# Optimization experiments

Hardware: AMD Instinct MI355X
Metric: run time of the kernel (lower is better)

The kernel has to match this reference:

```python
import jax, jax.numpy as jnp
import numpy as np

G = 8          # grid_size
N = G * G      # 64 nodes
DEG = 17       # neighbors per node for 8x8 sudoku (2x4 boxes)
STEPS = 32
H = 96         # hidden_dim
E = 16         # embed_size
B = 16         # batch


def sudoku_edges():
    # row (7) + col (7) + 2x4 box (7) neighbors, set-union -> 17 per node
    idx = np.arange(N).reshape(G, G)
    nb = []
    for j in range(N):
        r, c = j // G, j % G
        br, bc = (r // 2) * 2, (c // 4) * 4
        s = set(idx[r, :].tolist()) | set(idx[:, c].tolist()) | set(idx[br:br + 2, bc:bc + 4].flatten().tolist())
        s.discard(j)
        nb.append(sorted(s))
    return np.asarray(nb, dtype=np.int32)  # [64, 17]


def setup_inputs() -> dict:
    key = jax.random.key(0)
    ks = jax.random.split(key, 16)
    sc = 0.05
    inp = {
        "x": jax.random.randint(ks[0], (B, G, G), 0, G + 1),            # given digits, 0 = blank
        "target": jax.random.randint(ks[1], (B, G, G), 0, G) + 1,       # solutions in 1..8
        "edges": jnp.asarray(sudoku_edges()),                            # [64, 17] int32
        "digit_emb": jax.random.normal(ks[2], (G + 1, E), jnp.float32) * sc,
        "row_emb": jax.random.normal(ks[3], (G, E), jnp.float32) * sc,
        "col_emb": jax.random.normal(ks[4], (G, E), jnp.float32) * sc,
        "in0_W": jax.random.normal(ks[5], (3 * E, H), jnp.float32) * sc,
        "in0_b": jnp.zeros((H,), jnp.float32),
        "in_Ws": jax.random.normal(ks[6], (3, H, H), jnp.float32) * sc,
        "in_bs": jnp.zeros((3, H), jnp.float32),
        "msg0_W": jax.random.normal(ks[7], (2 * H, H), jnp.float32) * sc,
        "msg0_b": jnp.zeros((H,), jnp.float32),
        "msg_Ws": jax.random.normal(ks[8], (3, H, H), jnp.float32) * sc,
        "msg_bs": jnp.zeros((3, H), jnp.float32),
        "W_ih": jax.random.normal(ks[9], (2 * H, 4 * H), jnp.float32) * sc,
        "W_hh": jax.random.normal(ks[10], (H, 4 * H), jnp.float32) * sc,
        "b_ih": jnp.zeros((4 * H,), jnp.float32),
        "b_hh": jnp.zeros((4 * H,), jnp.float32),
        "pred_W": jax.random.normal(ks[11], (H, G), jnp.float32) * sc,
        "pred_b": jnp.zeros((G,), jnp.float32),
    }
    return inp


def _mlp(z, W0, b0, Ws, bs):
    # Linear -> ReLU -> Linear -> ReLU -> Linear -> ReLU -> Linear (def_MLP)
    z = jax.nn.relu(z @ W0 + b0)
    z = jax.nn.relu(z @ Ws[0] + bs[0])
    z = jax.nn.relu(z @ Ws[1] + bs[1])
    return z @ Ws[2] + bs[2]


def reference(x, target, edges, digit_emb, row_emb, col_emb,
              in0_W, in0_b, in_Ws, in_bs,
              msg0_W, msg0_b, msg_Ws, msg_bs,
              W_ih, W_hh, b_ih, b_hh, pred_W, pred_b):
    bsz = x.shape[0]
    xf = x.reshape(bsz, N)
    tgt = target.reshape(bsz, N) - 1                      # labels 0..7

    de = digit_emb[xf]                                    # [B,64,E]
    re = row_emb[jnp.repeat(jnp.arange(G), G)]            # [64,E]
    ce = col_emb[jnp.tile(jnp.arange(G), G)]              # [64,E]
    feat = jnp.concatenate([de,
                            jnp.broadcast_to(re[None], (bsz, N, E)),
                            jnp.broadcast_to(ce[None], (bsz, N, E))], axis=-1)
    xin = _mlp(feat, in0_W, in0_b, in_Ws, in_bs)          # [B,64,H]

    h0 = jnp.zeros((bsz, N, H), jnp.float32)
    s0 = jnp.zeros((bsz * N, H), jnp.float32)

    def step(carry, _):
        h, s, loss = carry
        # gather-by-edge message passing
        h_edges = h[:, edges]                                             # [B,64,17,H]
        h_self = jnp.broadcast_to(h[:, :, None, :], (bsz, N, DEG, H))
        msg = _mlp(jnp.concatenate([h_edges, h_self], -1),
                   msg0_W, msg0_b, msg_Ws, msg_bs).sum(axis=2)            # [B,64,H]
        # LSTMCell update
        lstm_in = jnp.concatenate([msg, xin], -1).reshape(bsz * N, 2 * H)
        gates = lstm_in @ W_ih + b_ih + h.reshape(bsz * N, H) @ W_hh + b_hh
        i, f, g, o = jnp.split(gates, 4, axis=-1)
        s2 = jax.nn.sigmoid(f) * s + jax.nn.sigmoid(i) * jnp.tanh(g)
        h2 = (jax.nn.sigmoid(o) * jnp.tanh(s2)).reshape(bsz, N, H)
        # per-step prediction / loss / accuracy
        logp = jax.nn.log_softmax(h2 @ pred_W + pred_b, axis=-1)          # [B,64,8]
        pred = jnp.argmax(logp, axis=-1)
        acc = jnp.mean(jnp.all(pred == tgt, axis=1).astype(jnp.float32))
        loss_n = -jnp.sum(jnp.take_along_axis(logp, tgt[..., None], -1)) / (bsz * N)
        return (h2, s2, loss + loss_n), acc

    (h, s, loss), accs = jax.lax.scan(step, (h0, s0, jnp.float32(0.0)), None, length=STEPS)
    loss = loss / STEPS
    final_pred = jnp.argmax(h @ pred_W + pred_b, axis=-1)                 # [B,64]
    return loss, accs, final_pred
```

## Files before the change

kernel.cpp:

```cpp
#include <hip/hip_runtime.h>

#define DEG 17
#define NSTEPS 32
#define HD 96
#define BB 16
#define NN 64
#define NODES (BB*NN)
#define Z1STR 80
#define Z2STR 84

#define WS_H      0
#define WS_S      98304
#define WS_U0     196608
#define WS_U1     393216
#define WS_XIN    590352
#define WS_GX     688656
#define WS_W1P    1081872
#define WS_W2P    1094160
#define WS_LOSSP  1106448
#define WS_CNTP   1114640

__global__ void wpad_kernel(const float* __restrict__ msg_Ws,
                            float* __restrict__ W1p, float* __restrict__ W2p)
{
  const int k = blockIdx.x;
  const int tid = threadIdx.x;
  const int jg = tid >> 3, jj = tid & 7;
  float v1 = 0.f, v2 = 0.f;
  if (jj < 6) {
    v1 = msg_Ws[k*96 + jg*6 + jj];
    v2 = msg_Ws[9216 + k*96 + jg*6 + jj];
  }
  W1p[k*128 + tid] = v1;
  W2p[k*128 + tid] = v2;
}

__global__ void init_kernel(
    const int* __restrict__ x,
    const float* __restrict__ digit_emb,
    const float* __restrict__ row_emb,
    const float* __restrict__ col_emb,
    const float* __restrict__ in0_W,
    const float* __restrict__ in0_b,
    const float* __restrict__ in_Ws,
    const float* __restrict__ in_bs,
    float* __restrict__ xin)
{
  const int node = blockIdx.x;
  const int j = threadIdx.x;
  const int n = node & 63;
  const int r = n >> 3, c = n & 7;
  __shared__ float feat[48];
  __shared__ float za[HD];
  __shared__ float zb[HD];
  if (j < 16)      feat[j] = digit_emb[x[node]*16 + j];
  else if (j < 32) feat[j] = row_emb[r*16 + (j-16)];
  else if (j < 48) feat[j] = col_emb[c*16 + (j-32)];
  __syncthreads();
  float a = in0_b[j];
  for (int k = 0; k < 48; ++k) a = fmaf(feat[k], in0_W[k*HD + j], a);
  za[j] = fmaxf(a, 0.f);
  __syncthreads();
  a = in_bs[j];
  for (int k = 0; k < HD; ++k) a = fmaf(za[k], in_Ws[k*HD + j], a);
  zb[j] = fmaxf(a, 0.f);
  __syncthreads();
  a = in_bs[HD + j];
  for (int k = 0; k < HD; ++k) a = fmaf(zb[k], in_Ws[9216 + k*HD + j], a);
  za[j] = fmaxf(a, 0.f);
  __syncthreads();
  a = in_bs[2*HD + j];
  for (int k = 0; k < HD; ++k) a = fmaf(za[k], in_Ws[2*9216 + k*HD + j], a);
  xin[node*HD + j] = a;
}

__global__ __launch_bounds__(384) void gx_kernel(
    const float* __restrict__ xin, const float* __restrict__ W_ih,
    const float* __restrict__ b_ih, const float* __restrict__ b_hh,
    float* __restrict__ gx)
{
  __shared__ float xs[4*HD];
  const int tid = threadIdx.x;
  const int base = blockIdx.x * 4;
  {
    const int m = tid / HD, k = tid - m*HD;
    xs[m*HD + k] = xin[(base+m)*HD + k];
  }
  __syncthreads();
  const int j = tid;
  float a0 = b_ih[j] + b_hh[j], a1 = a0, a2 = a0, a3 = a0;
  for (int k = 0; k < HD; ++k) {
    const float w = W_ih[(96+k)*384 + j];
    a0 = fmaf(xs[k], w, a0);
    a1 = fmaf(xs[HD+k], w, a1);
    a2 = fmaf(xs[2*HD+k], w, a2);
    a3 = fmaf(xs[3*HD+k], w, a3);
  }
  gx[(base+0)*384 + j] = a0;
  gx[(base+1)*384 + j] = a1;
  gx[(base+2)*384 + j] = a2;
  gx[(base+3)*384 + j] = a3;
}

__global__ __launch_bounds__(384) void step_kernel(
    const float* __restrict__ u_prev, float* __restrict__ u_next,
    float* __restrict__ h, float* __restrict__ s,
    const float* __restrict__ gx,
    const int* __restrict__ edges,
    const float* __restrict__ W1p, const float* __restrict__ W2p,
    const float* __restrict__ msg0_W, const float* __restrict__ msg0_b,
    const float* __restrict__ msg_Ws, const float* __restrict__ msg_bs,
    const float* __restrict__ W_ih, const float* __restrict__ W_hh,
    const float* __restrict__ pred_W, const float* __restrict__ pred_b,
    const int* __restrict__ target,
    float* __restrict__ lossP, int* __restrict__ cntP,
    float* __restrict__ final_pred_out, int step)
{
  __shared__ float sm[15744];
  float* const z1s = sm;
  float* const z2s = sm + 7680;
  float* const s3t   = sm;
  float* const msgh  = sm + 384;
  float* const h2t   = sm + 1152;
  float* const lgt   = sm + 1536;
  float* const gates = sm + 1568;
  float* const P3    = sm + 3104;
  float* const PL = z2s;
  float* const PU = z2s;

  const int tid = threadIdx.x;
  const int blk = blockIdx.x;
  const int base = blk * 4;
  const int bb = blk >> 4;
  const int nbase = (blk & 15) * 4;

  {
    const int m = tid / HD, k = tid - m*HD;
    const float usv = u_prev[(base+m)*192 + 96 + k];
    const float b0v = msg0_b[k];
    z1s[k*Z1STR + m*20 + 17] = 0.f;
    z1s[k*Z1STR + m*20 + 18] = 0.f;
    z1s[k*Z1STR + m*20 + 19] = 0.f;
    const int erow = (nbase + m) * DEG;
    #pragma unroll 1
    for (int r = 0; r < DEG; ++r) {
      const int nbr = edges[erow + r];
      const float ue = u_prev[(bb*64 + nbr)*192 + k];
      z1s[k*Z1STR + m*20 + r] = fmaxf(ue + usv + b0v, 0.f);
    }
  }
  __syncthreads();

  if (tid < 320) {
    const int jg = tid & 15, dg = tid >> 4;
    const int j6 = jg*6, j8 = jg*8, dg4 = dg*4;
    float acc[4][6];
    #pragma unroll
    for (int dd = 0; dd < 4; ++dd)
      #pragma unroll
      for (int jj = 0; jj < 6; ++jj) acc[dd][jj] = 0.f;
    #pragma unroll 4
    for (int k = 0; k < HD; ++k) {
      const float4 z = *(const float4*)&z1s[k*Z1STR + dg4];
      const float* wp = W1p + k*128 + j8;
      const float4 wa = *(const float4*)wp;
      const float2 wb = *(const float2*)(wp + 4);
      const float ze[4] = {z.x, z.y, z.z, z.w};
      const float we[6] = {wa.x, wa.y, wa.z, wa.w, wb.x, wb.y};
      #pragma unroll
      for (int dd = 0; dd < 4; ++dd)
        #pragma unroll
        for (int jj = 0; jj < 6; ++jj)
          acc[dd][jj] = fmaf(ze[dd], we[jj], acc[dd][jj]);
    }
    #pragma unroll
    for (int jj = 0; jj < 6; ++jj) {
      const float b1 = msg_bs[j6 + jj];
      float4 q;
      q.x = fmaxf(acc[0][jj] + b1, 0.f);
      q.y = fmaxf(acc[1][jj] + b1, 0.f);
      q.z = fmaxf(acc[2][jj] + b1, 0.f);
      q.w = fmaxf(acc[3][jj] + b1, 0.f);
      *(float4*)&z2s[(j6+jj)*Z2STR + dg4] = q;
    }
  }
  __syncthreads();

  {
    s3t[tid] = 0.f;
    const int m = tid / HD, k = tid - m*HD;
    msgh[(96+k)*4 + m] = h[(base+m)*HD + k];
  }
  __syncthreads();

  if (tid < 320) {
    const int jg = tid & 15, dg = tid >> 4;
    const int j6 = jg*6, j8 = jg*8, dg4 = dg*4;
    const int nd = dg / 5, dgl = dg - nd*5;
    float acc[4][6];
    #pragma unroll
    for (int dd = 0; dd < 4; ++dd)
      #pragma unroll
      for (int jj = 0; jj < 6; ++jj) acc[dd][jj] = 0.f;
    #pragma unroll 4
    for (int k = 0; k < HD; ++k) {
      const float4 z = *(const float4*)&z2s[k*Z2STR + dg4];
      const float* wp = W2p + k*128 + j8;
      const float4 wa = *(const float4*)wp;
      const float2 wb = *(const float2*)(wp + 4);
      const float ze[4] = {z.x, z.y, z.z, z.w};
      const float we[6] = {wa.x, wa.y, wa.z, wa.w, wb.x, wb.y};
      #pragma unroll
      for (int dd = 0; dd < 4; ++dd)
        #pragma unroll
        for (int jj = 0; jj < 6; ++jj)
          acc[dd][jj] = fmaf(ze[dd], we[jj], acc[dd][jj]);
    }
    const int nvalid = (dgl < 4) ? 4 : 1;
    #pragma unroll
    for (int jj = 0; jj < 6; ++jj) {
      const float b2 = msg_bs[96 + j6 + jj];
      float p = 0.f;
      #pragma unroll
      for (int dd = 0; dd < 4; ++dd)
        if (dd < nvalid) p += fmaxf(acc[dd][jj] + b2, 0.f);
      atomicAdd(&s3t[(j6+jj)*4 + nd], p);
    }
  }
  __syncthreads();

  if (tid < 192) {
    const int jg = tid % 24, kq = tid / 24;
    const int j4 = jg*4, k0 = kq*12;
    const float* W3 = msg_Ws + 2*9216;
    float acc[4][4];
    #pragma unroll
    for (int m = 0; m < 4; ++m)
      #pragma unroll
      for (int jj = 0; jj < 4; ++jj) acc[m][jj] = 0.f;
    #pragma unroll 4
    for (int kk = 0; kk < 12; ++kk) {
      const int k = k0 + kk;
      const float4 sv = *(const float4*)&s3t[k*4];
      const float4 wv = *(const float4*)&W3[k*96 + j4];
      const float se[4] = {sv.x, sv.y, sv.z, sv.w};
      const float we[4] = {wv.x, wv.y, wv.z, wv.w};
      #pragma unroll
      for (int m = 0; m < 4; ++m)
        #pragma unroll
        for (int jj = 0; jj < 4; ++jj)
          acc[m][jj] = fmaf(se[m], we[jj], acc[m][jj]);
    }
    #pragma unroll
    for (int m = 0; m < 4; ++m) {
      float4 q = {acc[m][0], acc[m][1], acc[m][2], acc[m][3]};
      *(float4*)&P3[(kq*4 + m)*96 + j4] = q;
    }
  }
  __syncthreads();
  {
    const int m = tid / HD, j = tid - m*HD;
    float v = 17.f * msg_bs[192 + j];
    #pragma unroll
    for (int kq = 0; kq < 8; ++kq) v += P3[(kq*4 + m)*96 + j];
    msgh[j*4 + m] = v;
  }
  __syncthreads();

  if (tid < 192) {
    const int jg = tid % 48, kq = tid / 48;
    const int j8 = jg*8, k0 = kq*48;
    const float* Wb = (kq < 2) ? (W_ih + j8) : (W_hh + j8 - 96*384);
    float acc[4][8];
    #pragma unroll
    for (int m = 0; m < 4; ++m)
      #pragma unroll
      for (int jj = 0; jj < 8; ++jj) acc[m][jj] = 0.f;
    #pragma unroll 2
    for (int k = k0; k < k0 + 48; ++k) {
      const float4 iv = *(const float4*)&msgh[k*4];
      const float* wp = Wb + k*384;
      const float4 wa = *(const float4*)wp;
      const float4 wc = *(const float4*)(wp + 4);
      const float ie[4] = {iv.x, iv.y, iv.z, iv.w};
      const float we[8] = {wa.x, wa.y, wa.z, wa.w, wc.x, wc.y, wc.z, wc.w};
      #pragma unroll
      for (int m = 0; m < 4; ++m)
        #pragma unroll
        for (int jj = 0; jj < 8; ++jj)
          acc[m][jj] = fmaf(ie[m], we[jj], acc[m][jj]);
    }
    #pragma unroll
    for (int m = 0; m < 4; ++m) {
      float4 qa = {acc[m][0], acc[m][1], acc[m][2], acc[m][3]};
      float4 qb = {acc[m][4], acc[m][5], acc[m][6], acc[m][7]};
      *(float4*)&PL[(kq*4 + m)*384 + j8] = qa;
      *(float4*)&PL[(kq*4 + m)*384 + j8 + 4] = qb;
    }
  }
  __syncthreads();
  {
    const int j = tid;
    #pragma unroll
    for (int m = 0; m < 4; ++m) {
      float g = gx[(base+m)*384 + j];
      #pragma unroll
      for (int kq = 0; kq < 4; ++kq) g += PL[(kq*4 + m)*384 + j];
      gates[m*384 + j] = g;
    }
  }
  __syncthreads();

  {
    const int m = tid / HD, hj = tid - m*HD;
    const int node = base + m;
    const float gi = gates[m*384 + hj];
    const float gf = gates[m*384 + 96 + hj];
    const float gg = gates[m*384 + 192 + hj];
    const float go = gates[m*384 + 288 + hj];
    const float sv = s[node*HD + hj];
    const float ig = 1.f/(1.f + expf(-gi));
    const float fg = 1.f/(1.f + expf(-gf));
    const float cg = tanhf(gg);
    const float og = 1.f/(1.f + expf(-go));
    const float s2 = fg*sv + ig*cg;
    const float h2 = og*tanhf(s2);
    s[node*HD + hj] = s2;
    h[node*HD + hj] = h2;
    h2t[hj*4 + m] = h2;
  }
  __syncthreads();

  if (tid < 192) {
    const int jg = tid % 24, kq = tid / 24;
    const int j8 = jg*8, k0 = kq*12;
    const float* Wb = (j8 < 96) ? (msg0_W + j8) : (msg0_W + 9216 + j8 - 96);
    float acc[4][8];
    #pragma unroll
    for (int m = 0; m < 4; ++m)
      #pragma unroll
      for (int jj = 0; jj < 8; ++jj) acc[m][jj] = 0.f;
    #pragma unroll 4
    for (int kk = 0; kk < 12; ++kk) {
      const int k = k0 + kk;
      const float4 iv = *(const float4*)&h2t[k*4];
      const float* wp = Wb + k*96;
      const float4 wa = *(const float4*)wp;
      const float4 wc = *(const float4*)(wp + 4);
      const float ie[4] = {iv.x, iv.y, iv.z, iv.w};
      const float we[8] = {wa.x, wa.y, wa.z, wa.w, wc.x, wc.y, wc.z, wc.w};
      #pragma unroll
      for (int m = 0; m < 4; ++m)
        #pragma unroll
        for (int jj = 0; jj < 8; ++jj)
          acc[m][jj] = fmaf(ie[m], we[jj], acc[m][jj]);
    }
    #pragma unroll
    for (int m = 0; m < 4; ++m) {
      float4 qa = {acc[m][0], acc[m][1], acc[m][2], acc[m][3]};
      float4 qb = {acc[m][4], acc[m][5], acc[m][6], acc[m][7]};
      *(float4*)&PU[(kq*4 + m)*192 + j8] = qa;
      *(float4*)&PU[(kq*4 + m)*192 + j8 + 4] = qb;
    }
  }
  __syncthreads();
  {
    const int j = tid % 192, mh = tid / 192;
    #pragma unroll
    for (int t = 0; t < 2; ++t) {
      const int mm = mh + 2*t;
      float v = 0.f;
      #pragma unroll
      for (int kq = 0; kq < 8; ++kq) v += PU[(kq*4 + mm)*192 + j];
      u_next[(base+mm)*192 + j] = v;
    }
  }

  if (tid < 256) {
    const int m = tid >> 6, c = (tid >> 3) & 7, kq = tid & 7;
    float p = 0.f;
    #pragma unroll
    for (int kk = 0; kk < 12; ++kk) {
      const int k = kq*12 + kk;
      p = fmaf(h2t[k*4 + m], pred_W[k*8 + c], p);
    }
    p += __shfl_xor(p, 1);
    p += __shfl_xor(p, 2);
    p += __shfl_xor(p, 4);
    if (kq == 0) lgt[m*8 + c] = p + pred_b[c];
  }
  __syncthreads();
  if (tid < 4) {
    const int m = tid;
    const int node = base + m;
    float mx = lgt[m*8];
    int pred = 0;
    #pragma unroll
    for (int c = 1; c < 8; ++c) {
      const float v = lgt[m*8 + c];
      if (v > mx) { mx = v; pred = c; }
    }
    float sum = 0.f;
    #pragma unroll
    for (int c = 0; c < 8; ++c) sum += expf(lgt[m*8 + c] - mx);
    const float lse = mx + logf(sum);
    const int tgt = target[node] - 1;
    lgt[16 + m] = lse - lgt[m*8 + tgt];
    lgt[20 + m] = (pred == tgt) ? 1.f : 0.f;
    if (step == NSTEPS-1) final_pred_out[node] = (float)pred;
    if (m == 0) {
      lossP[step*256 + blk] = lgt[16] + lgt[17] + lgt[18] + lgt[19];
      cntP[step*256 + blk] = (int)(lgt[20] + lgt[21] + lgt[22] + lgt[23]);
    }
  }
}

__global__ void finalize_kernel(const float* __restrict__ lossP,
                                const int* __restrict__ cntP,
                                float* __restrict__ out)
{
  __shared__ float sl[32];
  const int tid = threadIdx.x;
  const int st = tid >> 3, q = tid & 7;
  float lsum = 0.f;
  for (int i = 0; i < 32; ++i) lsum += lossP[st*256 + q*32 + i];
  lsum += __shfl_xor(lsum, 1);
  lsum += __shfl_xor(lsum, 2);
  lsum += __shfl_xor(lsum, 4);
  if (q == 0) sl[st] = lsum;
  float okc = 0.f;
  #pragma unroll
  for (int t = 0; t < 2; ++t) {
    const int bbat = q + 8*t;
    int c = 0;
    for (int i = 0; i < 16; ++i) c += cntP[st*256 + bbat*16 + i];
    okc += (c == 64) ? 1.f : 0.f;
  }
  okc += __shfl_xor(okc, 1);
  okc += __shfl_xor(okc, 2);
  okc += __shfl_xor(okc, 4);
  if (q == 0) out[1 + st] = okc / 16.f;
  __syncthreads();
  if (tid == 0) {
    float tot = 0.f;
    for (int i = 0; i < 32; ++i) tot += sl[i];
    out[0] = tot / ((float)NODES * (float)NSTEPS);
  }
}

extern "C" void kernel_launch(void* const* d_in, const int* in_sizes, int n_in,
                              void* d_out, int out_size, void* d_ws, size_t ws_size,
                              hipStream_t stream) {
  const int*   x         = (const int*)  d_in[0];
  const int*   target    = (const int*)  d_in[1];
  const int*   edges     = (const int*)  d_in[2];
  const float* digit_emb = (const float*)d_in[3];
  const float* row_emb   = (const float*)d_in[4];
  const float* col_emb   = (const float*)d_in[5];
  const float* in0_W     = (const float*)d_in[6];
  const float* in0_b     = (const float*)d_in[7];
  const float* in_Ws     = (const float*)d_in[8];
  const float* in_bs     = (const float*)d_in[9];
  const float* msg0_W    = (const float*)d_in[10];
  const float* msg0_b    = (const float*)d_in[11];
  const float* msg_Ws    = (const float*)d_in[12];
  const float* msg_bs    = (const float*)d_in[13];
  const float* W_ih      = (const float*)d_in[14];
  const float* W_hh      = (const float*)d_in[15];
  const float* pred_W    = (const float*)d_in[18];
  const float* pred_b    = (const float*)d_in[19];

  float* ws    = (float*)d_ws;
  float* hbuf  = ws + WS_H;
  float* sbuf  = ws + WS_S;
  float* u0    = ws + WS_U0;
  float* u1    = ws + WS_U1;
  float* xin   = ws + WS_XIN;
  float* gxb   = ws + WS_GX;
  float* W1p   = ws + WS_W1P;
  float* W2p   = ws + WS_W2P;
  float* lossP = ws + WS_LOSSP;
  int*   cntP  = (int*)(ws + WS_CNTP);

  hipMemsetAsync(d_ws, 0, (size_t)393216*sizeof(float), stream);

  wpad_kernel<<<96, 128, 0, stream>>>(msg_Ws, W1p, W2p);
  init_kernel<<<NODES, HD, 0, stream>>>(x, digit_emb, row_emb, col_emb,
                                        in0_W, in0_b, in_Ws, in_bs, xin);
  gx_kernel<<<256, 384, 0, stream>>>(xin, W_ih,
                                     (const float*)d_in[16], (const float*)d_in[17],
                                     gxb);

  float* outp = (float*)d_out;
  for (int st = 0; st < NSTEPS; ++st) {
    const float* up = (st & 1) ? u1 : u0;
    float*       un = (st & 1) ? u0 : u1;
    step_kernel<<<256, 384, 0, stream>>>(
        up, un, hbuf, sbuf, gxb, edges,
        W1p, W2p, msg0_W, msg0_b, msg_Ws, msg_bs,
        W_ih, W_hh, pred_W, pred_b,
        target, lossP, cntP, outp + 1 + NSTEPS, st);
  }

  finalize_kernel<<<1, 256, 0, stream>>>(lossP, cntP, outp);
}
```

Before: 1.170 ms.

## Split step kernel to two nodes per block across 512 blocks

The per-step kernel now handles two nodes per block instead of four and launches 512 blocks, so more workgroups run at once on the many CUs of the device. The padded weight layout and thread mappings are reworked (3 outputs per thread, split-K reductions over more partial slices), and msg0_b is folded into the u buffer so the gather no longer adds it. Loss partials are moved to reuse the xin region. The cost is more partial-sum reduction work per node and more blocks re-reading the weights.

```diff
diff --git a/kernel.cpp b/kernel.cpp
--- a/kernel.cpp
+++ b/kernel.cpp
@@ -6,8 +6,7 @@
 #define BB 16
 #define NN 64
 #define NODES (BB*NN)
-#define Z1STR 80
-#define Z2STR 84
+#define NBLK 512
 
 #define WS_H      0
 #define WS_S      98304
@@ -17,19 +16,19 @@
 #define WS_GX     688656
 #define WS_W1P    1081872
 #define WS_W2P    1094160
-#define WS_LOSSP  1106448
-#define WS_CNTP   1114640
+#define WS_LOSSP  WS_XIN
+#define WS_CNTP   (WS_XIN + 16384)
 
 __global__ void wpad_kernel(const float* __restrict__ msg_Ws,
                             float* __restrict__ W1p, float* __restrict__ W2p)
 {
   const int k = blockIdx.x;
   const int tid = threadIdx.x;
-  const int jg = tid >> 3, jj = tid & 7;
+  const int jg = tid >> 2, jj = tid & 3;
   float v1 = 0.f, v2 = 0.f;
-  if (jj < 6) {
-    v1 = msg_Ws[k*96 + jg*6 + jj];
-    v2 = msg_Ws[9216 + k*96 + jg*6 + jj];
+  if (jj < 3) {
+    v1 = msg_Ws[k*96 + jg*3 + jj];
+    v2 = msg_Ws[9216 + k*96 + jg*3 + jj];
   }
   W1p[k*128 + tid] = v1;
   W2p[k*128 + tid] = v2;
@@ -44,7 +43,9 @@
     const float* __restrict__ in0_b,
     const float* __restrict__ in_Ws,
     const float* __restrict__ in_bs,
-    float* __restrict__ xin)
+    const float* __restrict__ msg0_b,
+    float* __restrict__ xin,
+    float* __restrict__ u0)
 {
   const int node = blockIdx.x;
   const int j = threadIdx.x;
@@ -56,6 +57,7 @@
   if (j < 16)      feat[j] = digit_emb[x[node]*16 + j];
   else if (j < 32) feat[j] = row_emb[r*16 + (j-16)];
   else if (j < 48) feat[j] = col_emb[c*16 + (j-32)];
+  u0[node*192 + 96 + j] = msg0_b[j];
   __syncthreads();
   float a = in0_b[j];
   for (int k = 0; k < 48; ++k) a = fmaf(feat[k], in0_W[k*HD + j], a);
@@ -102,7 +104,7 @@
   gx[(base+3)*384 + j] = a3;
 }
 
-__global__ __launch_bounds__(384) void step_kernel(
+__global__ __launch_bounds__(384, 3) void step_kernel(
     const float* __restrict__ u_prev, float* __restrict__ u_next,
     float* __restrict__ h, float* __restrict__ s,
     const float* __restrict__ gx,
@@ -116,203 +118,205 @@
     float* __restrict__ lossP, int* __restrict__ cntP,
     float* __restrict__ final_pred_out, int step)
 {
-  __shared__ float sm[15744];
-  float* const z1s = sm;
-  float* const z2s = sm + 7680;
-  float* const s3t   = sm;
-  float* const msgh  = sm + 384;
-  float* const h2t   = sm + 1152;
-  float* const lgt   = sm + 1536;
-  float* const gates = sm + 1568;
-  float* const P3    = sm + 3104;
-  float* const PL = z2s;
-  float* const PU = z2s;
+  __shared__ float sm[15392];
+  float* const z1s   = sm;
+  float* const z2s   = sm + 3840;
+  float* const pp    = sm + 7680;
+  float* const s3t   = sm + 13824;
+  float* const msgh  = sm + 14016;
+  float* const h2t   = sm + 14400;
+  float* const gates = sm + 14592;
+  float* const lgt   = sm + 15360;
 
   const int tid = threadIdx.x;
   const int blk = blockIdx.x;
-  const int base = blk * 4;
-  const int bb = blk >> 4;
-  const int nbase = (blk & 15) * 4;
-
-  {
-    const int m = tid / HD, k = tid - m*HD;
-    const float usv = u_prev[(base+m)*192 + 96 + k];
-    const float b0v = msg0_b[k];
-    z1s[k*Z1STR + m*20 + 17] = 0.f;
-    z1s[k*Z1STR + m*20 + 18] = 0.f;
-    z1s[k*Z1STR + m*20 + 19] = 0.f;
-    const int erow = (nbase + m) * DEG;
-    #pragma unroll 1
-    for (int r = 0; r < DEG; ++r) {
-      const int nbr = edges[erow + r];
-      const float ue = u_prev[(bb*64 + nbr)*192 + k];
-      z1s[k*Z1STR + m*20 + r] = fmaxf(ue + usv + b0v, 0.f);
-    }
-  }
-  __syncthreads();
+  const int base = blk * 2;
+  const int bb = blk >> 5;
+  const int nbase = (blk & 31) * 2;
 
   if (tid < 320) {
-    const int jg = tid & 15, dg = tid >> 4;
-    const int j6 = jg*6, j8 = jg*8, dg4 = dg*4;
-    float acc[4][6];
+    const int row = tid % 40;
+    const int kh  = tid / 40;
+    const int m = row / 20, r = row % 20;
+    const int k0 = kh * 12;
+    if (r < DEG) {
+      const int nbr = edges[(nbase + m)*DEG + r];
+      const float* uep = u_prev + (bb*64 + nbr)*192 + k0;
+      const float* usp = u_prev + (base + m)*192 + 96 + k0;
+      #pragma unroll
+      for (int t = 0; t < 3; ++t) {
+        const float4 ue = *(const float4*)(uep + 4*t);
+        const float4 us = *(const float4*)(usp + 4*t);
+        z1s[(k0 + 4*t + 0)*40 + row] = fmaxf(ue.x + us.x, 0.f);
+        z1s[(k0 + 4*t + 1)*40 + row] = fmaxf(ue.y + us.y, 0.f);
+        z1s[(k0 + 4*t + 2)*40 + row] = fmaxf(ue.z + us.z, 0.f);
+        z1s[(k0 + 4*t + 3)*40 + row] = fmaxf(ue.w + us.w, 0.f);
+      }
+    } else {
+      #pragma unroll
+      for (int t = 0; t < 12; ++t) z1s[(k0 + t)*40 + row] = 0.f;
+    }
+  }
+  if (tid < 192) {
+    s3t[tid] = 0.f;
+  } else {
+    const int i = tid - 192;
+    const int m2 = i / 96, k2 = i % 96;
+    msgh[(96 + k2)*2 + m2] = h[(base + m2)*HD + k2];
+  }
+  __syncthreads();
+
+  if (tid < 320) {
+    const int jg = tid & 31, dg = tid >> 5;
+    const int j3 = jg*3;
+    float acc[4][3];
     #pragma unroll
     for (int dd = 0; dd < 4; ++dd)
       #pragma unroll
-      for (int jj = 0; jj < 6; ++jj) acc[dd][jj] = 0.f;
+      for (int jj = 0; jj < 3; ++jj) acc[dd][jj] = 0.f;
     #pragma unroll 4
     for (int k = 0; k < HD; ++k) {
-      const float4 z = *(const float4*)&z1s[k*Z1STR + dg4];
-      const float* wp = W1p + k*128 + j8;
-      const float4 wa = *(const float4*)wp;
-      const float2 wb = *(const float2*)(wp + 4);
+      const float4 z = *(const float4*)&z1s[k*40 + dg*4];
+      const float4 w = *(const float4*)&W1p[k*128 + jg*4];
       const float ze[4] = {z.x, z.y, z.z, z.w};
-      const float we[6] = {wa.x, wa.y, wa.z, wa.w, wb.x, wb.y};
+      const float we[3] = {w.x, w.y, w.z};
       #pragma unroll
       for (int dd = 0; dd < 4; ++dd)
         #pragma unroll
-        for (int jj = 0; jj < 6; ++jj)
+        for (int jj = 0; jj < 3; ++jj)
           acc[dd][jj] = fmaf(ze[dd], we[jj], acc[dd][jj]);
     }
     #pragma unroll
-    for (int jj = 0; jj < 6; ++jj) {
-      const float b1 = msg_bs[j6 + jj];
+    for (int jj = 0; jj < 3; ++jj) {
+      const float b1 = msg_bs[j3 + jj];
       float4 q;
       q.x = fmaxf(acc[0][jj] + b1, 0.f);
       q.y = fmaxf(acc[1][jj] + b1, 0.f);
       q.z = fmaxf(acc[2][jj] + b1, 0.f);
       q.w = fmaxf(acc[3][jj] + b1, 0.f);
-      *(float4*)&z2s[(j6+jj)*Z2STR + dg4] = q;
-    }
-  }
-  __syncthreads();
-
-  {
-    s3t[tid] = 0.f;
-    const int m = tid / HD, k = tid - m*HD;
-    msgh[(96+k)*4 + m] = h[(base+m)*HD + k];
+      *(float4*)&z2s[(j3+jj)*40 + dg*4] = q;
+    }
   }
   __syncthreads();
 
   if (tid < 320) {
-    const int jg = tid & 15, dg = tid >> 4;
-    const int j6 = jg*6, j8 = jg*8, dg4 = dg*4;
+    const int jg = tid & 31, dg = tid >> 5;
+    const int j3 = jg*3;
     const int nd = dg / 5, dgl = dg - nd*5;
-    float acc[4][6];
+    float acc[4][3];
     #pragma unroll
     for (int dd = 0; dd < 4; ++dd)
       #pragma unroll
-      for (int jj = 0; jj < 6; ++jj) acc[dd][jj] = 0.f;
+      for (int jj = 0; jj < 3; ++jj) acc[dd][jj] = 0.f;
     #pragma unroll 4
     for (int k = 0; k < HD; ++k) {
-      const float4 z = *(const float4*)&z2s[k*Z2STR + dg4];
-      const float* wp = W2p + k*128 + j8;
-      const float4 wa = *(const float4*)wp;
-      const float2 wb = *(const float2*)(wp + 4);
+      const float4 z = *(const float4*)&z2s[k*40 + dg*4];
+      const float4 w = *(const float4*)&W2p[k*128 + jg*4];
       const float ze[4] = {z.x, z.y, z.z, z.w};
-      const float we[6] = {wa.x, wa.y, wa.z, wa.w, wb.x, wb.y};
+      const float we[3] = {w.x, w.y, w.z};
       #pragma unroll
       for (int dd = 0; dd < 4; ++dd)
         #pragma unroll
-        for (int jj = 0; jj < 6; ++jj)
+        for (int jj = 0; jj < 3; ++jj)
           acc[dd][jj] = fmaf(ze[dd], we[jj], acc[dd][jj]);
     }
     const int nvalid = (dgl < 4) ? 4 : 1;
     #pragma unroll
-    for (int jj = 0; jj < 6; ++jj) {
-      const float b2 = msg_bs[96 + j6 + jj];
+    for (int jj = 0; jj < 3; ++jj) {
+      const float b2 = msg_bs[96 + j3 + jj];
       float p = 0.f;
       #pragma unroll
       for (int dd = 0; dd < 4; ++dd)
         if (dd < nvalid) p += fmaxf(acc[dd][jj] + b2, 0.f);
-      atomicAdd(&s3t[(j6+jj)*4 + nd], p);
-    }
-  }
-  __syncthreads();
-
-  if (tid < 192) {
+      atomicAdd(&s3t[(j3+jj)*2 + nd], p);
+    }
+  }
+  __syncthreads();
+
+  {
     const int jg = tid % 24, kq = tid / 24;
-    const int j4 = jg*4, k0 = kq*12;
+    const int j4 = jg*4, k0 = kq*6;
     const float* W3 = msg_Ws + 2*9216;
-    float acc[4][4];
-    #pragma unroll
-    for (int m = 0; m < 4; ++m)
+    float acc[2][4];
+    #pragma unroll
+    for (int m = 0; m < 2; ++m)
       #pragma unroll
       for (int jj = 0; jj < 4; ++jj) acc[m][jj] = 0.f;
-    #pragma unroll 4
-    for (int kk = 0; kk < 12; ++kk) {
+    #pragma unroll
+    for (int kk = 0; kk < 6; ++kk) {
       const int k = k0 + kk;
-      const float4 sv = *(const float4*)&s3t[k*4];
+      const float2 sv = *(const float2*)&s3t[k*2];
       const float4 wv = *(const float4*)&W3[k*96 + j4];
-      const float se[4] = {sv.x, sv.y, sv.z, sv.w};
+      const float se[2] = {sv.x, sv.y};
       const float we[4] = {wv.x, wv.y, wv.z, wv.w};
       #pragma unroll
-      for (int m = 0; m < 4; ++m)
+      for (int m = 0; m < 2; ++m)
         #pragma unroll
         for (int jj = 0; jj < 4; ++jj)
           acc[m][jj] = fmaf(se[m], we[jj], acc[m][jj]);
     }
     #pragma unroll
-    for (int m = 0; m < 4; ++m) {
+    for (int m = 0; m < 2; ++m) {
       float4 q = {acc[m][0], acc[m][1], acc[m][2], acc[m][3]};
-      *(float4*)&P3[(kq*4 + m)*96 + j4] = q;
-    }
-  }
-  __syncthreads();
+      *(float4*)&pp[(kq*2 + m)*96 + j4] = q;
+    }
+  }
+  __syncthreads();
+  if (tid < 192) {
+    const int m = tid / 96, j = tid % 96;
+    float v = 17.f * msg_bs[192 + j];
+    #pragma unroll
+    for (int kq = 0; kq < 16; ++kq) v += pp[(kq*2 + m)*96 + j];
+    msgh[j*2 + m] = v;
+  }
+  __syncthreads();
+
   {
-    const int m = tid / HD, j = tid - m*HD;
-    float v = 17.f * msg_bs[192 + j];
-    #pragma unroll
-    for (int kq = 0; kq < 8; ++kq) v += P3[(kq*4 + m)*96 + j];
-    msgh[j*4 + m] = v;
-  }
-  __syncthreads();
-
-  if (tid < 192) {
     const int jg = tid % 48, kq = tid / 48;
-    const int j8 = jg*8, k0 = kq*48;
-    const float* Wb = (kq < 2) ? (W_ih + j8) : (W_hh + j8 - 96*384);
-    float acc[4][8];
-    #pragma unroll
-    for (int m = 0; m < 4; ++m)
+    const int j8 = jg*8, k0 = kq*24;
+    const float* Wb = (kq < 4) ? (W_ih + j8) : (W_hh + j8 - 96*384);
+    float acc[2][8];
+    #pragma unroll
+    for (int m = 0; m < 2; ++m)
       #pragma unroll
       for (int jj = 0; jj < 8; ++jj) acc[m][jj] = 0.f;
     #pragma unroll 2
-    for (int k = k0; k < k0 + 48; ++k) {
-      const float4 iv = *(const float4*)&msgh[k*4];
+    for (int k = k0; k < k0 + 24; ++k) {
+      const float2 iv = *(const float2*)&msgh[k*2];
       const float* wp = Wb + k*384;
       const float4 wa = *(const float4*)wp;
       const float4 wc = *(const float4*)(wp + 4);
-      const float ie[4] = {iv.x, iv.y, iv.z, iv.w};
+      const float ie[2] = {iv.x, iv.y};
       const float we[8] = {wa.x, wa.y, wa.z, wa.w, wc.x, wc.y, wc.z, wc.w};
       #pragma unroll
-      for (int m = 0; m < 4; ++m)
+      for (int m = 0; m < 2; ++m)
         #pragma unroll
         for (int jj = 0; jj < 8; ++jj)
           acc[m][jj] = fmaf(ie[m], we[jj], acc[m][jj]);
     }
     #pragma unroll
-    for (int m = 0; m < 4; ++m) {
+    for (int m = 0; m < 2; ++m) {
       float4 qa = {acc[m][0], acc[m][1], acc[m][2], acc[m][3]};
       float4 qb = {acc[m][4], acc[m][5], acc[m][6], acc[m][7]};
-      *(float4*)&PL[(kq*4 + m)*384 + j8] = qa;
-      *(float4*)&PL[(kq*4 + m)*384 + j8 + 4] = qb;
+      *(float4*)&pp[(kq*2 + m)*384 + j8]     = qa;
+      *(float4*)&pp[(kq*2 + m)*384 + j8 + 4] = qb;
     }
   }
   __syncthreads();
   {
     const int j = tid;
     #pragma unroll
-    for (int m = 0; m < 4; ++m) {
+    for (int m = 0; m < 2; ++m) {
       float g = gx[(base+m)*384 + j];
       #pragma unroll
-      for (int kq = 0; kq < 4; ++kq) g += PL[(kq*4 + m)*384 + j];
+      for (int kq = 0; kq < 8; ++kq) g += pp[(kq*2 + m)*384 + j];
       gates[m*384 + j] = g;
     }
   }
   __syncthreads();
 
-  {
-    const int m = tid / HD, hj = tid - m*HD;
+  if (tid < 192) {
+    const int m = tid / 96, hj = tid % 96;
     const int node = base + m;
     const float gi = gates[m*384 + hj];
     const float gf = gates[m*384 + 96 + hj];
@@ -327,62 +331,58 @@
     const float h2 = og*tanhf(s2);
     s[node*HD + hj] = s2;
     h[node*HD + hj] = h2;
-    h2t[hj*4 + m] = h2;
-  }
-  __syncthreads();
-
-  if (tid < 192) {
+    h2t[hj*2 + m] = h2;
+  }
+  __syncthreads();
+
+  {
     const int jg = tid % 24, kq = tid / 24;
-    const int j8 = jg*8, k0 = kq*12;
+    const int j8 = jg*8, k0 = kq*6;
     const float* Wb = (j8 < 96) ? (msg0_W + j8) : (msg0_W + 9216 + j8 - 96);
-    float acc[4][8];
-    #pragma unroll
-    for (int m = 0; m < 4; ++m)
+    float acc[2][8];
+    #pragma unroll
+    for (int m = 0; m < 2; ++m)
       #pragma unroll
       for (int jj = 0; jj < 8; ++jj) acc[m][jj] = 0.f;
-    #pragma unroll 4
-    for (int kk = 0; kk < 12; ++kk) {
+    #pragma unroll
+    for (int kk = 0; kk < 6; ++kk) {
       const int k = k0 + kk;
-      const float4 iv = *(const float4*)&h2t[k*4];
+      const float2 iv = *(const float2*)&h2t[k*2];
       const float* wp = Wb + k*96;
       const float4 wa = *(const float4*)wp;
       const float4 wc = *(const float4*)(wp + 4);
-      const float ie[4] = {iv.x, iv.y, iv.z, iv.w};
+      const float ie[2] = {iv.x, iv.y};
       const float we[8] = {wa.x, wa.y, wa.z, wa.w, wc.x, wc.y, wc.z, wc.w};
       #pragma unroll
-      for (int m = 0; m < 4; ++m)
+      for (int m = 0; m < 2; ++m)
         #pragma unroll
         for (int jj = 0; jj < 8; ++jj)
           acc[m][jj] = fmaf(ie[m], we[jj], acc[m][jj]);
     }
     #pragma unroll
-    for (int m = 0; m < 4; ++m) {
+    for (int m = 0; m < 2; ++m) {
       float4 qa = {acc[m][0], acc[m][1], acc[m][2], acc[m][3]};
       float4 qb = {acc[m][4], acc[m][5], acc[m][6], acc[m][7]};
-      *(float4*)&PU[(kq*4 + m)*192 + j8] = qa;
-      *(float4*)&PU[(kq*4 + m)*192 + j8 + 4] = qb;
+      *(float4*)&pp[(kq*2 + m)*192 + j8]     = qa;
+      *(float4*)&pp[(kq*2 + m)*192 + j8 + 4] = qb;
     }
   }
   __syncthreads();
   {
-    const int j = tid % 192, mh = tid / 192;
-    #pragma unroll
-    for (int t = 0; t < 2; ++t) {
-      const int mm = mh + 2*t;
-      float v = 0.f;
-      #pragma unroll
-      for (int kq = 0; kq < 8; ++kq) v += PU[(kq*4 + mm)*192 + j];
-      u_next[(base+mm)*192 + j] = v;
-    }
-  }
-
-  if (tid < 256) {
+    const int j = tid % 192, m = tid / 192;
+    float v = (j >= 96) ? msg0_b[j - 96] : 0.f;
+    #pragma unroll
+    for (int kq = 0; kq < 16; ++kq) v += pp[(kq*2 + m)*192 + j];
+    u_next[(base+m)*192 + j] = v;
+  }
+
+  if (tid < 128) {
     const int m = tid >> 6, c = (tid >> 3) & 7, kq = tid & 7;
     float p = 0.f;
     #pragma unroll
     for (int kk = 0; kk < 12; ++kk) {
       const int k = kq*12 + kk;
-      p = fmaf(h2t[k*4 + m], pred_W[k*8 + c], p);
+      p = fmaf(h2t[k*2 + m], pred_W[k*8 + c], p);
     }
     p += __shfl_xor(p, 1);
     p += __shfl_xor(p, 2);
@@ -390,7 +390,7 @@
     if (kq == 0) lgt[m*8 + c] = p + pred_b[c];
   }
   __syncthreads();
-  if (tid < 4) {
+  if (tid < 2) {
     const int m = tid;
     const int node = base + m;
     float mx = lgt[m*8];
@@ -406,11 +406,11 @@
     const float lse = mx + logf(sum);
     const int tgt = target[node] - 1;
     lgt[16 + m] = lse - lgt[m*8 + tgt];
-    lgt[20 + m] = (pred == tgt) ? 1.f : 0.f;
+    lgt[18 + m] = (pred == tgt) ? 1.f : 0.f;
     if (step == NSTEPS-1) final_pred_out[node] = (float)pred;
     if (m == 0) {
-      lossP[step*256 + blk] = lgt[16] + lgt[17] + lgt[18] + lgt[19];
-      cntP[step*256 + blk] = (int)(lgt[20] + lgt[21] + lgt[22] + lgt[23]);
+      lossP[step*NBLK + blk] = lgt[16] + lgt[17];
+      cntP[step*NBLK + blk] = (int)(lgt[18] + lgt[19]);
     }
   }
 }
@@ -423,7 +423,7 @@
   const int tid = threadIdx.x;
   const int st = tid >> 3, q = tid & 7;
   float lsum = 0.f;
-  for (int i = 0; i < 32; ++i) lsum += lossP[st*256 + q*32 + i];
+  for (int i = 0; i < 64; ++i) lsum += lossP[st*NBLK + q*64 + i];
   lsum += __shfl_xor(lsum, 1);
   lsum += __shfl_xor(lsum, 2);
   lsum += __shfl_xor(lsum, 4);
@@ -433,7 +433,7 @@
   for (int t = 0; t < 2; ++t) {
     const int bbat = q + 8*t;
     int c = 0;
-    for (int i = 0; i < 16; ++i) c += cntP[st*256 + bbat*16 + i];
+    for (int i = 0; i < 32; ++i) c += cntP[st*NBLK + bbat*32 + i];
     okc += (c == 64) ? 1.f : 0.f;
   }
   okc += __shfl_xor(okc, 1);
@@ -486,7 +486,8 @@
 
   wpad_kernel<<<96, 128, 0, stream>>>(msg_Ws, W1p, W2p);
   init_kernel<<<NODES, HD, 0, stream>>>(x, digit_emb, row_emb, col_emb,
-                                        in0_W, in0_b, in_Ws, in_bs, xin);
+                                        in0_W, in0_b, in_Ws, in_bs,
+                                        msg0_b, xin, u0);
   gx_kernel<<<256, 384, 0, stream>>>(xin, W_ih,
                                      (const float*)d_in[16], (const float*)d_in[17],
                                      gxb);
@@ -495,7 +496,7 @@
   for (int st = 0; st < NSTEPS; ++st) {
     const float* up = (st & 1) ? u1 : u0;
     float*       un = (st & 1) ? u0 : u1;
-    step_kernel<<<256, 384, 0, stream>>>(
+    step_kernel<<<NBLK, 384, 0, stream>>>(
         up, un, hbuf, sbuf, gxb, edges,
         W1p, W2p, msg0_W, msg0_b, msg_Ws, msg_bs,
         W_ih, W_hh, pred_W, pred_b,
```

New measurement: 1.371 ms. 17.2% more time.
